# Performance work log

Measured on AMD Instinct MI355X. Metric: run time of the kernel, lower is better.

The kernel has to match this reference:

```python
import jax, jax.numpy as jnp
import numpy as np

FEAT = 1024     # args.gl_text_dim
BERT_DIM = 768
EPS = 1e-12     # torch F.normalize eps


def _conv_branch(x, W, b):
    # x: (bs, L, 768); W: (FEAT, K, 768); b: (FEAT,)
    # Equivalent to Conv2d(1, FEAT, (K, 768)) then relu, already transposed to (bs, L-K+1, FEAT)
    K = W.shape[1]
    L = x.shape[1]
    out = sum(jnp.einsum('bld,fd->blf', x[:, k:L - K + 1 + k, :], W[:, k, :]) for k in range(K))
    return jax.nn.relu(out + b)


def _l2norm(x, axis):
    n = jnp.sqrt(jnp.sum(x * x, axis=axis, keepdims=True))
    return x / jnp.maximum(n, EPS)


def setup_inputs() -> dict:
    key = jax.random.key(0)
    ks = jax.random.split(key, 10)
    bs, L = 128, 128
    def w(k, shape, fan_in):
        bound = 1.0 / np.sqrt(fan_in)
        return jax.random.uniform(k, shape, jnp.float32, -bound, bound)
    return {
        'words_emb': jax.random.normal(ks[0], (bs, L, BERT_DIM), jnp.float32),
        'sent_emb': jax.random.normal(ks[1], (bs, BERT_DIM), jnp.float32),
        'W2': w(ks[2], (FEAT, 2, BERT_DIM), 2 * BERT_DIM), 'b2': w(ks[3], (FEAT,), 2 * BERT_DIM),
        'W3': w(ks[4], (FEAT, 3, BERT_DIM), 3 * BERT_DIM), 'b3': w(ks[5], (FEAT,), 3 * BERT_DIM),
        'W4': w(ks[6], (FEAT, 4, BERT_DIM), 4 * BERT_DIM), 'b4': w(ks[7], (FEAT,), 4 * BERT_DIM),
        'Wp': w(ks[8], (FEAT, BERT_DIM), BERT_DIM), 'bp': w(ks[9], (FEAT,), BERT_DIM),
    }


def reference(words_emb, sent_emb, W2, b2, W3, b3, W4, b4, Wp, bp):
    # sentence head: dropout(eval=identity) -> linear -> l2 normalize
    sent = _l2norm(sent_emb @ Wp.T + bp, axis=-1)  # (bs, FEAT)

    L = words_emb.shape[1]  # == bert_words_num
    a = _conv_branch(words_emb, W2, b2)  # (bs, L-1, FEAT)
    b_ = _conv_branch(words_emb, W3, b3)  # (bs, L-2, FEAT)
    c = _conv_branch(words_emb, W4, b4)  # (bs, L-3, FEAT)

    seq = L - 1 - 3  # args.bert_words_num - 1 - 3
    main = jnp.maximum(jnp.maximum(a[:, :seq], b_[:, :seq]), c[:, :seq])  # (bs, seq, FEAT)
    pen = jnp.maximum(a[:, seq], b_[:, seq])[:, None]                      # (bs, 1, FEAT)
    last = a[:, seq + 1][:, None]                                          # (bs, 1, FEAT)
    code = jnp.concatenate([main, pen, last], axis=1)                      # (bs, L-2, FEAT)
    code = _l2norm(code, axis=2)
    words_out = jnp.transpose(code, (0, 2, 1))                             # (bs, FEAT, L-2)
    return words_out, sent
```

## Files before the change

kernel.cpp:

```cpp
#include <hip/hip_runtime.h>
#include <math.h>

typedef unsigned short u16;

#define BSZ 128
#define SEQL 128
#define DIM 768
#define FEAT 1024
#define WORDS_OUT_ELEMS (BSZ * FEAT * 126)

typedef __attribute__((ext_vector_type(8))) __bf16 bf16x8;
typedef __attribute__((ext_vector_type(4))) float f32x4;

__device__ __forceinline__ u16 f2bf(float x) {
  unsigned u = __float_as_uint(x);
  u += 0x7FFFu + ((u >> 16) & 1u);
  return (u16)(u >> 16);
}

__device__ __forceinline__ void gld_lds16(const void* g, void* l) {
  __builtin_amdgcn_global_load_lds(
      (const __attribute__((address_space(1))) void*)g,
      (__attribute__((address_space(3))) void*)l, 16, 0, 0);
}

#define N4_WORDS 3145728
#define N4_W2 393216
#define N4_W3 589824
#define N4_W4 786432
#define N4_TOTAL (N4_WORDS + N4_W2 + N4_W3 + N4_W4)

__global__ __launch_bounds__(256) void cvt_all(const float* __restrict__ words,
                                               const float* __restrict__ W2,
                                               const float* __restrict__ W3,
                                               const float* __restrict__ W4,
                                               u16* __restrict__ dA, u16* __restrict__ d2,
                                               u16* __restrict__ d3, u16* __restrict__ d4) {
  int i = blockIdx.x * 256 + threadIdx.x;
  if (i >= N4_TOTAL) return;
  const float* src;
  u16* dst;
  int j = i;
  if (j < N4_WORDS) {
    src = words; dst = dA;
  } else if ((j -= N4_WORDS) < N4_W2) {
    src = W2; dst = d2;
  } else if ((j -= N4_W2) < N4_W3) {
    src = W3; dst = d3;
  } else {
    j -= N4_W3; src = W4; dst = d4;
  }
  float4 v = ((const float4*)src)[j];
  ushort4 o;
  o.x = f2bf(v.x); o.y = f2bf(v.y); o.z = f2bf(v.z); o.w = f2bf(v.w);
  ((ushort4*)dst)[j] = o;
}

__device__ __forceinline__ void stage_tile(const u16* __restrict__ gbase, int stride,
                                           u16* __restrict__ ldsbase, int wave, int lane) {
#pragma unroll
  for (int i = 0; i < 4; ++i) {
    int slot = i * 256 + wave * 64 + lane;
    int r = slot >> 3, c = slot & 7;
    const u16* src = gbase + (size_t)r * stride + ((c ^ (r & 7)) * 8);
    unsigned uofs = __builtin_amdgcn_readfirstlane((unsigned)((i * 256 + wave * 64) * 8));
    gld_lds16(src, ldsbase + uofs);
  }
}

template <int K>
__device__ __forceinline__ void run_branch(const u16* __restrict__ A,
                                           const u16* __restrict__ W,
                                           const float* __restrict__ bias,
                                           u16* __restrict__ C,
                                           int b0, int tile_n, u16* lds) {
  const int KD = K * 768;
  const int Lp = 129 - K;
  const int tid = threadIdx.x;
  const int wave = tid >> 6, lane = tid & 63;
  u16* Xs = lds;
  u16* Wb0 = lds + 16384;
  u16* Wb1 = lds + 24576;

  const int bsel = wave & 1;
  const int wm = bsel * 128;
  const int wn = (wave >> 1) * 64;
  const int frow = lane & 15;
  const int fq = lane >> 4;

  const u16* xg0 = A + (size_t)b0 * 128 * 768;
  const u16* xg1 = A + (size_t)(b0 + 1) * 128 * 768;
  const u16* wg = W + (size_t)tile_n * 128 * KD;

  f32x4 acc[8][4];
#pragma unroll
  for (int mi = 0; mi < 8; ++mi)
#pragma unroll
    for (int ni = 0; ni < 4; ++ni) acc[mi][ni] = 0.0f;

  for (int d0 = 0; d0 < 768; d0 += 64) {
    stage_tile(xg0 + d0, 768, Xs, wave, lane);
    stage_tile(xg1 + d0, 768, Xs + 8192, wave, lane);
    stage_tile(wg + d0, KD, Wb0, wave, lane);
    __syncthreads();
#pragma unroll
    for (int k = 0; k < K; ++k) {
      if (k + 1 < K)
        stage_tile(wg + (k + 1) * 768 + d0, KD, ((k + 1) & 1) ? Wb1 : Wb0, wave, lane);
      const u16* wbuf = (k & 1) ? Wb1 : Wb0;
#pragma unroll
      for (int kc = 0; kc < 2; ++kc) {
        bf16x8 af[8], wf[4];
#pragma unroll
        for (int mi = 0; mi < 8; ++mi) {
          int row = wm + mi * 16 + frow + k;
          af[mi] = *(const bf16x8*)&Xs[(row * 8 + ((kc * 4 + fq) ^ (row & 7))) * 8];
        }
#pragma unroll
        for (int ni = 0; ni < 4; ++ni) {
          int row = wn + ni * 16 + frow;
          wf[ni] = *(const bf16x8*)&wbuf[(row * 8 + ((kc * 4 + fq) ^ (row & 7))) * 8];
        }
#pragma unroll
        for (int mi = 0; mi < 8; ++mi)
#pragma unroll
          for (int ni = 0; ni < 4; ++ni)
            acc[mi][ni] = __builtin_amdgcn_mfma_f32_16x16x32_bf16(af[mi], wf[ni],
                                                                  acc[mi][ni], 0, 0, 0);
      }
      __syncthreads();
    }
  }

  float bv[4];
#pragma unroll
  for (int ni = 0; ni < 4; ++ni) bv[ni] = bias[tile_n * 128 + wn + ni * 16 + frow];
  const int bb = b0 + bsel;
#pragma unroll
  for (int mi = 0; mi < 8; ++mi) {
#pragma unroll
    for (int r = 0; r < 4; ++r) {
      int mg = mi * 16 + fq * 4 + r;
      if (mg < Lp) {
        ushort4 hs;
        hs.x = f2bf(fmaxf(acc[mi][0][r] + bv[0], 0.0f));
        hs.y = f2bf(fmaxf(acc[mi][1][r] + bv[1], 0.0f));
        hs.z = f2bf(fmaxf(acc[mi][2][r] + bv[2], 0.0f));
        hs.w = f2bf(fmaxf(acc[mi][3][r] + bv[3], 0.0f));
        *(ushort4*)(C + (size_t)(bb * Lp + mg) * FEAT + tile_n * 128 + wn + frow * 4) = hs;
      }
    }
  }
}

__global__ __launch_bounds__(256, 2) void gemm_fused(const u16* __restrict__ A,
                                                     const u16* __restrict__ W2,
                                                     const u16* __restrict__ W3,
                                                     const u16* __restrict__ W4,
                                                     const float* __restrict__ b2,
                                                     const float* __restrict__ b3,
                                                     const float* __restrict__ b4,
                                                     u16* __restrict__ Ca,
                                                     u16* __restrict__ Cb,
                                                     u16* __restrict__ Cc) {
  __shared__ u16 lds[32768];
  const int tile_n = blockIdx.x;
  const int z = blockIdx.y;
  const int b0 = blockIdx.z * 2;
  if (z == 0)
    run_branch<2>(A, W2, b2, Ca, b0, tile_n, lds);
  else if (z == 1)
    run_branch<3>(A, W3, b3, Cb, b0, tile_n, lds);
  else
    run_branch<4>(A, W4, b4, Cc, b0, tile_n, lds);
}

__device__ __forceinline__ float4 load_bf4(const u16* p) {
  uint2 q = *(const uint2*)p;
  float4 r;
  r.x = __uint_as_float((q.x & 0xFFFFu) << 16);
  r.y = __uint_as_float(q.x & 0xFFFF0000u);
  r.z = __uint_as_float((q.y & 0xFFFFu) << 16);
  r.w = __uint_as_float(q.y & 0xFFFF0000u);
  return r;
}

#define CSTR 1028

__global__ __launch_bounds__(256) void combine_norm(const u16* __restrict__ a,
                                                    const u16* __restrict__ b,
                                                    const u16* __restrict__ c,
                                                    float* __restrict__ out) {
  __shared__ float comb[16 * CSTR];
  __shared__ float red[16 * 4];
  __shared__ float inv[16];
  const int tid = threadIdx.x;
  const int wave = tid >> 6, lane = tid & 63;
  const int l0 = blockIdx.x * 16;
  const int bb = blockIdx.y;
  const int rem = (126 - l0 < 16) ? (126 - l0) : 16;
  const int f0 = tid * 4;
  const int chunk = tid >> 4, frow = tid & 15;
  const int fbase = chunk * 64 + frow;

  float part[16];
#pragma unroll
  for (int l = 0; l < 16; ++l) {
    int lg = l0 + l;
    float4 v = make_float4(0.f, 0.f, 0.f, 0.f);
    if (lg < 126) {
      v = load_bf4(a + (size_t)(bb * 127 + lg) * 1024 + f0);
      if (lg < 125) {
        float4 vb = load_bf4(b + (size_t)(bb * 126 + lg) * 1024 + f0);
        v.x = fmaxf(v.x, vb.x); v.y = fmaxf(v.y, vb.y);
        v.z = fmaxf(v.z, vb.z); v.w = fmaxf(v.w, vb.w);
      }
      if (lg < 124) {
        float4 vc = load_bf4(c + (size_t)(bb * 125 + lg) * 1024 + f0);
        v.x = fmaxf(v.x, vc.x); v.y = fmaxf(v.y, vc.y);
        v.z = fmaxf(v.z, vc.z); v.w = fmaxf(v.w, vc.w);
      }
    }
    comb[l * CSTR + fbase + 0] = v.x;
    comb[l * CSTR + fbase + 16] = v.y;
    comb[l * CSTR + fbase + 32] = v.z;
    comb[l * CSTR + fbase + 48] = v.w;
    part[l] = v.x * v.x + v.y * v.y + v.z * v.z + v.w * v.w;
  }
#pragma unroll
  for (int l = 0; l < 16; ++l) {
    float v = part[l];
    for (int off = 32; off > 0; off >>= 1) v += __shfl_down(v, off);
    if (lane == 0) red[l * 4 + wave] = v;
  }
  __syncthreads();
  if (tid < 16) {
    float s = red[tid * 4] + red[tid * 4 + 1] + red[tid * 4 + 2] + red[tid * 4 + 3];
    inv[tid] = 1.0f / fmaxf(sqrtf(s), 1e-12f);
  }
  __syncthreads();

  const int q = lane & 3, fi = lane >> 2;
  const int lb = 4 * q;
  const size_t ob = (size_t)bb * FEAT * 126;
#pragma unroll
  for (int it = 0; it < 16; ++it) {
    int f = wave * 256 + it * 16 + fi;
    if (lb + 2 <= rem) {
      float* po = out + ob + (size_t)f * 126 + l0 + lb;
      float2 w0;
      w0.x = comb[(lb + 0) * CSTR + f] * inv[lb + 0];
      w0.y = comb[(lb + 1) * CSTR + f] * inv[lb + 1];
      *(float2*)po = w0;
      if (lb + 4 <= rem) {
        float2 w1;
        w1.x = comb[(lb + 2) * CSTR + f] * inv[lb + 2];
        w1.y = comb[(lb + 3) * CSTR + f] * inv[lb + 3];
        *(float2*)(po + 2) = w1;
      }
    }
  }
}

__global__ __launch_bounds__(256) void sent_head(const float* __restrict__ se,
                                                 const float* __restrict__ Wp,
                                                 const float* __restrict__ bp,
                                                 float* __restrict__ out) {
  __shared__ float srow[768];
  __shared__ float ov[1024];
  __shared__ float red[4];
  const int b = blockIdx.x, tid = threadIdx.x;
  for (int i = tid; i < 768; i += 256) srow[i] = se[b * 768 + i];
  __syncthreads();
  float ss = 0.f;
#pragma unroll
  for (int it = 0; it < 4; ++it) {
    int f = tid + it * 256;
    const float4* w = (const float4*)(Wp + (size_t)f * 768);
    float acc = 0.f;
    for (int j = 0; j < 192; ++j) {
      float4 wv = w[j];
      float4 sv = *(const float4*)&srow[j * 4];
      acc += wv.x * sv.x + wv.y * sv.y + wv.z * sv.z + wv.w * sv.w;
    }
    acc += bp[f];
    ov[f] = acc;
    ss += acc * acc;
  }
  const int lane = tid & 63, wave = tid >> 6;
  for (int off = 32; off > 0; off >>= 1) ss += __shfl_down(ss, off);
  if (lane == 0) red[wave] = ss;
  __syncthreads();
  float tot = red[0] + red[1] + red[2] + red[3];
  float inv = 1.0f / fmaxf(sqrtf(tot), 1e-12f);
  for (int it = 0; it < 4; ++it) {
    int f = tid + it * 256;
    out[WORDS_OUT_ELEMS + (size_t)b * 1024 + f] = ov[f] * inv;
  }
}

extern "C" void kernel_launch(void* const* d_in, const int* in_sizes, int n_in,
                              void* d_out, int out_size, void* d_ws, size_t ws_size,
                              hipStream_t stream) {
  const float* words = (const float*)d_in[0];
  const float* sent = (const float*)d_in[1];
  const float* W2 = (const float*)d_in[2];
  const float* b2 = (const float*)d_in[3];
  const float* W3 = (const float*)d_in[4];
  const float* b3 = (const float*)d_in[5];
  const float* W4 = (const float*)d_in[6];
  const float* b4 = (const float*)d_in[7];
  const float* Wp = (const float*)d_in[8];
  const float* bp = (const float*)d_in[9];
  float* out = (float*)d_out;

  char* ws = (char*)d_ws;
  u16* A_bf = (u16*)(ws + 0);
  u16* W2_bf = (u16*)(ws + 25165824);
  u16* W3_bf = (u16*)(ws + 28311552);
  u16* W4_bf = (u16*)(ws + 33030144);
  u16* a_out = (u16*)(ws + 39321600);
  u16* b_out = (u16*)(ws + 72613888);
  u16* c_out = (u16*)(ws + 105644032);

  cvt_all<<<(N4_TOTAL + 255) / 256, 256, 0, stream>>>(words, W2, W3, W4,
                                                      A_bf, W2_bf, W3_bf, W4_bf);

  gemm_fused<<<dim3(8, 3, BSZ / 2), 256, 0, stream>>>(A_bf, W2_bf, W3_bf, W4_bf,
                                                      b2, b3, b4, a_out, b_out, c_out);

  combine_norm<<<dim3(8, BSZ), 256, 0, stream>>>(a_out, b_out, c_out, out);
  sent_head<<<BSZ, 256, 0, stream>>>(sent, Wp, bp, out);
}
```

Baseline: 476.7 us.

## Enlarge conv GEMM tile to four batches per block with double-buffered X

Each block now covers four batch items, one per wave, with each wave holding a 128x128 output tile (8x8 MFMA fragments), where before each wave held 128x64. The X staging is double-buffered across the d-chunk loop, and the W stages form one continuous ping-pong pipeline across (d, k) steps. The goal is to halve W traffic per output and overlap X loads with compute. In exchange, LDS use rises to 160KB and accumulator registers double, dropping occupancy to one block per CU, and the grid shrinks to 768 blocks.

Result: slower. 690.9 us (+44.9%).

```diff
diff --git a/kernel.cpp b/kernel.cpp
--- a/kernel.cpp
+++ b/kernel.cpp
@@ -78,53 +78,65 @@
   const int Lp = 129 - K;
   const int tid = threadIdx.x;
   const int wave = tid >> 6, lane = tid & 63;
-  u16* Xs = lds;
-  u16* Wb0 = lds + 16384;
-  u16* Wb1 = lds + 24576;
-
-  const int bsel = wave & 1;
-  const int wm = bsel * 128;
-  const int wn = (wave >> 1) * 64;
+  u16* Xb0 = lds;
+  u16* Xb1 = lds + 32768;
+  u16* Wb0 = lds + 65536;
+  u16* Wb1 = lds + 73728;
+
   const int frow = lane & 15;
   const int fq = lane >> 4;
 
-  const u16* xg0 = A + (size_t)b0 * 128 * 768;
-  const u16* xg1 = A + (size_t)(b0 + 1) * 128 * 768;
+  const u16* xg = A + (size_t)b0 * 98304;
   const u16* wg = W + (size_t)tile_n * 128 * KD;
 
-  f32x4 acc[8][4];
+  f32x4 acc[8][8];
 #pragma unroll
   for (int mi = 0; mi < 8; ++mi)
 #pragma unroll
-    for (int ni = 0; ni < 4; ++ni) acc[mi][ni] = 0.0f;
-
-  for (int d0 = 0; d0 < 768; d0 += 64) {
-    stage_tile(xg0 + d0, 768, Xs, wave, lane);
-    stage_tile(xg1 + d0, 768, Xs + 8192, wave, lane);
-    stage_tile(wg + d0, KD, Wb0, wave, lane);
-    __syncthreads();
+    for (int ni = 0; ni < 8; ++ni) acc[mi][ni] = 0.0f;
+
+#pragma unroll
+  for (int q = 0; q < 4; ++q)
+    stage_tile(xg + (size_t)q * 98304, 768, Xb0 + q * 8192, wave, lane);
+  stage_tile(wg, KD, Wb0, wave, lane);
+  __syncthreads();
+
+  for (int d0i = 0; d0i < 12; ++d0i) {
+    const int dd = d0i * 64;
+    u16* Xcur = (d0i & 1) ? Xb1 : Xb0;
 #pragma unroll
     for (int k = 0; k < K; ++k) {
-      if (k + 1 < K)
-        stage_tile(wg + (k + 1) * 768 + d0, KD, ((k + 1) & 1) ? Wb1 : Wb0, wave, lane);
-      const u16* wbuf = (k & 1) ? Wb1 : Wb0;
+      const int s = d0i * K + k;
+      if (s + 1 < 12 * K) {
+        const int nk = (k + 1 < K) ? k + 1 : 0;
+        const int nd = (k + 1 < K) ? dd : dd + 64;
+        stage_tile(wg + nk * 768 + nd, KD, ((s + 1) & 1) ? Wb1 : Wb0, wave, lane);
+      }
+      if (k == K - 1 && d0i < 11) {
+        u16* Xn = (d0i & 1) ? Xb0 : Xb1;
+#pragma unroll
+        for (int q = 0; q < 4; ++q)
+          stage_tile(xg + (size_t)q * 98304 + dd + 64, 768, Xn + q * 8192, wave, lane);
+      }
+      const u16* xb = Xcur + wave * 8192;
+      const u16* wb = (s & 1) ? Wb1 : Wb0;
 #pragma unroll
       for (int kc = 0; kc < 2; ++kc) {
-        bf16x8 af[8], wf[4];
+        bf16x8 af[8], wf[8];
 #pragma unroll
         for (int mi = 0; mi < 8; ++mi) {
-          int row = wm + mi * 16 + frow + k;
-          af[mi] = *(const bf16x8*)&Xs[(row * 8 + ((kc * 4 + fq) ^ (row & 7))) * 8];
+          int row = mi * 16 + frow + k;
+          af[mi] = *(const bf16x8*)&xb[(row * 8 + ((kc * 4 + fq) ^ (row & 7))) * 8];
         }
 #pragma unroll
-        for (int ni = 0; ni < 4; ++ni) {
-          int row = wn + ni * 16 + frow;
-          wf[ni] = *(const bf16x8*)&wbuf[(row * 8 + ((kc * 4 + fq) ^ (row & 7))) * 8];
+        for (int ni = 0; ni < 8; ++ni) {
+          int row = ni * 16 + frow;
+          wf[ni] = *(const bf16x8*)&wb[(row * 8 + ((kc * 4 + fq) ^ (row & 7))) * 8];
         }
 #pragma unroll
         for (int mi = 0; mi < 8; ++mi)
 #pragma unroll
-          for (int ni = 0; ni < 4; ++ni)
+          for (int ni = 0; ni < 8; ++ni)
             acc[mi][ni] = __builtin_amdgcn_mfma_f32_16x16x32_bf16(af[mi], wf[ni],
                                                                   acc[mi][ni], 0, 0, 0);
       }
@@ -132,28 +144,34 @@
     }
   }
 
-  float bv[4];
-#pragma unroll
-  for (int ni = 0; ni < 4; ++ni) bv[ni] = bias[tile_n * 128 + wn + ni * 16 + frow];
-  const int bb = b0 + bsel;
+  float bv[8];
+#pragma unroll
+  for (int ni = 0; ni < 8; ++ni) bv[ni] = bias[tile_n * 128 + ni * 16 + frow];
+  const int bb = b0 + wave;
 #pragma unroll
   for (int mi = 0; mi < 8; ++mi) {
 #pragma unroll
     for (int r = 0; r < 4; ++r) {
       int mg = mi * 16 + fq * 4 + r;
       if (mg < Lp) {
-        ushort4 hs;
-        hs.x = f2bf(fmaxf(acc[mi][0][r] + bv[0], 0.0f));
-        hs.y = f2bf(fmaxf(acc[mi][1][r] + bv[1], 0.0f));
-        hs.z = f2bf(fmaxf(acc[mi][2][r] + bv[2], 0.0f));
-        hs.w = f2bf(fmaxf(acc[mi][3][r] + bv[3], 0.0f));
-        *(ushort4*)(C + (size_t)(bb * Lp + mg) * FEAT + tile_n * 128 + wn + frow * 4) = hs;
-      }
-    }
-  }
-}
-
-__global__ __launch_bounds__(256, 2) void gemm_fused(const u16* __restrict__ A,
+        ushort4 h0, h1;
+        h0.x = f2bf(fmaxf(acc[mi][0][r] + bv[0], 0.0f));
+        h0.y = f2bf(fmaxf(acc[mi][1][r] + bv[1], 0.0f));
+        h0.z = f2bf(fmaxf(acc[mi][2][r] + bv[2], 0.0f));
+        h0.w = f2bf(fmaxf(acc[mi][3][r] + bv[3], 0.0f));
+        h1.x = f2bf(fmaxf(acc[mi][4][r] + bv[4], 0.0f));
+        h1.y = f2bf(fmaxf(acc[mi][5][r] + bv[5], 0.0f));
+        h1.z = f2bf(fmaxf(acc[mi][6][r] + bv[6], 0.0f));
+        h1.w = f2bf(fmaxf(acc[mi][7][r] + bv[7], 0.0f));
+        u16* pc = C + (size_t)(bb * Lp + mg) * FEAT + tile_n * 128;
+        *(ushort4*)(pc + frow * 4) = h0;
+        *(ushort4*)(pc + 64 + frow * 4) = h1;
+      }
+    }
+  }
+}
+
+__global__ __launch_bounds__(256, 1) void gemm_fused(const u16* __restrict__ A,
                                                      const u16* __restrict__ W2,
                                                      const u16* __restrict__ W3,
                                                      const u16* __restrict__ W4,
@@ -163,10 +181,10 @@
                                                      u16* __restrict__ Ca,
                                                      u16* __restrict__ Cb,
                                                      u16* __restrict__ Cc) {
-  __shared__ u16 lds[32768];
+  __shared__ u16 lds[81920];
   const int tile_n = blockIdx.x;
   const int z = blockIdx.y;
-  const int b0 = blockIdx.z * 2;
+  const int b0 = blockIdx.z * 4;
   if (z == 0)
     run_branch<2>(A, W2, b2, Ca, b0, tile_n, lds);
   else if (z == 1)
@@ -326,7 +344,7 @@
   cvt_all<<<(N4_TOTAL + 255) / 256, 256, 0, stream>>>(words, W2, W3, W4,
                                                       A_bf, W2_bf, W3_bf, W4_bf);
 
-  gemm_fused<<<dim3(8, 3, BSZ / 2), 256, 0, stream>>>(A_bf, W2_bf, W3_bf, W4_bf,
+  gemm_fused<<<dim3(8, 3, BSZ / 4), 256, 0, stream>>>(A_bf, W2_bf, W3_bf, W4_bf,
                                                       b2, b3, b4, a_out, b_out, c_out);
 
   combine_norm<<<dim3(8, BSZ), 256, 0, stream>>>(a_out, b_out, c_out, out);
```

## Enlarge GEMM block to four batches with double-buffered X/W LDS pipeline

Applied to the files above, without the earlier changes.

The conv-GEMM block now covers four batch items with 512 threads, and the launch grid is halved along z. It stages the whole 64-wide X slice for all four batches into a double buffer and prefetches the next slice and the next W tile during compute. Waits now use explicit vmcnt counts and split MFMA phases with setprio and s_barrier instead of full __syncthreads. This aims to reuse each W tile across more rows and overlap global-to-LDS loads with MFMA work. The cost is 160KB of LDS per block, which allows one block per CU, plus fragile hand-tuned wait counts.

New measurement: 503.0 us. 1.06x slower.

```diff
diff --git a/kernel.cpp b/kernel.cpp
--- a/kernel.cpp
+++ b/kernel.cpp
@@ -23,6 +23,10 @@
       (const __attribute__((address_space(1))) void*)g,
       (__attribute__((address_space(3))) void*)l, 16, 0, 0);
 }
+
+#define WAITVM0 asm volatile("s_waitcnt vmcnt(0)" ::: "memory")
+#define WAITVM2 asm volatile("s_waitcnt vmcnt(2)" ::: "memory")
+#define WAITVM4 asm volatile("s_waitcnt vmcnt(4)" ::: "memory")
 
 #define N4_WORDS 3145728
 #define N4_W2 393216
@@ -56,17 +60,40 @@
   ((ushort4*)dst)[j] = o;
 }
 
-__device__ __forceinline__ void stage_tile(const u16* __restrict__ gbase, int stride,
-                                           u16* __restrict__ ldsbase, int wave, int lane) {
-#pragma unroll
-  for (int i = 0; i < 4; ++i) {
-    int slot = i * 256 + wave * 64 + lane;
+__device__ __forceinline__ void stage_tile512(const u16* __restrict__ gbase, int stride,
+                                              u16* __restrict__ ldsbase, int wave, int lane) {
+#pragma unroll
+  for (int p = 0; p < 2; ++p) {
+    int slot = p * 512 + wave * 64 + lane;
     int r = slot >> 3, c = slot & 7;
     const u16* src = gbase + (size_t)r * stride + ((c ^ (r & 7)) * 8);
-    unsigned uofs = __builtin_amdgcn_readfirstlane((unsigned)((i * 256 + wave * 64) * 8));
+    unsigned uofs = __builtin_amdgcn_readfirstlane((unsigned)((p * 512 + wave * 64) * 8));
     gld_lds16(src, ldsbase + uofs);
   }
 }
+
+#define GPHASE(kc, mh, WLOAD)                                                        \
+  {                                                                                  \
+    bf16x8 af[4];                                                                    \
+    _Pragma("unroll") for (int i = 0; i < 4; ++i) {                                  \
+      int row = (mh * 4 + i) * 16 + frow + k;                                        \
+      af[i] = *(const bf16x8*)&xb[(row * 8 + ((kc * 4 + fq) ^ (row & 7))) * 8];      \
+    }                                                                                \
+    if (WLOAD) {                                                                     \
+      _Pragma("unroll") for (int ni = 0; ni < 4; ++ni) {                             \
+        int row = wn + ni * 16 + frow;                                               \
+        wf[ni] = *(const bf16x8*)&wcur[(row * 8 + ((kc * 4 + fq) ^ (row & 7))) * 8]; \
+      }                                                                              \
+    }                                                                                \
+    __builtin_amdgcn_s_setprio(1);                                                   \
+    _Pragma("unroll") for (int i = 0; i < 4; ++i)                                    \
+        _Pragma("unroll") for (int ni = 0; ni < 4; ++ni)                             \
+            acc[mh * 4 + i][ni] = __builtin_amdgcn_mfma_f32_16x16x32_bf16(           \
+                af[i], wf[ni], acc[mh * 4 + i][ni], 0, 0, 0);                        \
+    __builtin_amdgcn_s_setprio(0);                                                   \
+    __builtin_amdgcn_sched_barrier(0);                                               \
+    __builtin_amdgcn_s_barrier();                                                    \
+  }
 
 template <int K>
 __device__ __forceinline__ void run_branch(const u16* __restrict__ A,
@@ -76,20 +103,15 @@
                                            int b0, int tile_n, u16* lds) {
   const int KD = K * 768;
   const int Lp = 129 - K;
+  const int S = 12 * K;
   const int tid = threadIdx.x;
   const int wave = tid >> 6, lane = tid & 63;
-  u16* Xs = lds;
-  u16* Wb0 = lds + 16384;
-  u16* Wb1 = lds + 24576;
-
-  const int bsel = wave & 1;
-  const int wm = bsel * 128;
-  const int wn = (wave >> 1) * 64;
   const int frow = lane & 15;
   const int fq = lane >> 4;
-
-  const u16* xg0 = A + (size_t)b0 * 128 * 768;
-  const u16* xg1 = A + (size_t)(b0 + 1) * 128 * 768;
+  const int wq = wave >> 1;
+  const int wn = (wave & 1) * 64;
+
+  const u16* xg = A + (size_t)b0 * 98304;
   const u16* wg = W + (size_t)tile_n * 128 * KD;
 
   f32x4 acc[8][4];
@@ -98,44 +120,50 @@
 #pragma unroll
     for (int ni = 0; ni < 4; ++ni) acc[mi][ni] = 0.0f;
 
-  for (int d0 = 0; d0 < 768; d0 += 64) {
-    stage_tile(xg0 + d0, 768, Xs, wave, lane);
-    stage_tile(xg1 + d0, 768, Xs + 8192, wave, lane);
-    stage_tile(wg + d0, KD, Wb0, wave, lane);
-    __syncthreads();
+#pragma unroll
+  for (int q = 0; q < 4; ++q)
+    stage_tile512(xg + (size_t)q * 98304, 768, lds + q * 8192, wave, lane);
+  stage_tile512(wg, KD, lds + 65536, wave, lane);
+  WAITVM0;
+  __builtin_amdgcn_sched_barrier(0);
+  __syncthreads();
+
+  for (int d0i = 0; d0i < 12; ++d0i) {
+    const int dd = d0i * 64;
+    u16* Xcur = (d0i & 1) ? (lds + 32768) : lds;
+    u16* Xnxt = (d0i & 1) ? lds : (lds + 32768);
+    const u16* xb = Xcur + wq * 8192;
 #pragma unroll
     for (int k = 0; k < K; ++k) {
-      if (k + 1 < K)
-        stage_tile(wg + (k + 1) * 768 + d0, KD, ((k + 1) & 1) ? Wb1 : Wb0, wave, lane);
-      const u16* wbuf = (k & 1) ? Wb1 : Wb0;
-#pragma unroll
-      for (int kc = 0; kc < 2; ++kc) {
-        bf16x8 af[8], wf[4];
-#pragma unroll
-        for (int mi = 0; mi < 8; ++mi) {
-          int row = wm + mi * 16 + frow + k;
-          af[mi] = *(const bf16x8*)&Xs[(row * 8 + ((kc * 4 + fq) ^ (row & 7))) * 8];
-        }
-#pragma unroll
-        for (int ni = 0; ni < 4; ++ni) {
-          int row = wn + ni * 16 + frow;
-          wf[ni] = *(const bf16x8*)&wbuf[(row * 8 + ((kc * 4 + fq) ^ (row & 7))) * 8];
-        }
-#pragma unroll
-        for (int mi = 0; mi < 8; ++mi)
-#pragma unroll
-          for (int ni = 0; ni < 4; ++ni)
-            acc[mi][ni] = __builtin_amdgcn_mfma_f32_16x16x32_bf16(af[mi], wf[ni],
-                                                                  acc[mi][ni], 0, 0, 0);
-      }
-      __syncthreads();
+      const int s = d0i * K + k;
+      const bool lastk = (k == K - 1);
+      const bool stx = lastk && (d0i < 11);
+      u16* wcur = (s & 1) ? (lds + 73728) : (lds + 65536);
+      u16* wnxt = (s & 1) ? (lds + 65536) : (lds + 73728);
+      const int nk = lastk ? 0 : k + 1;
+      const int nd = lastk ? dd + 64 : dd;
+
+      if (s + 1 < S) stage_tile512(wg + nk * 768 + nd, KD, wnxt, wave, lane);
+      if (stx) stage_tile512(xg + dd + 64, 768, Xnxt, wave, lane);
+      if (s + 1 == S) { WAITVM0; } else if (stx) { WAITVM4; } else { WAITVM2; }
+      __builtin_amdgcn_sched_barrier(0);
+      __builtin_amdgcn_s_barrier();
+
+      bf16x8 wf[4];
+      GPHASE(0, 0, 1)
+      if (stx) stage_tile512(xg + 98304 + dd + 64, 768, Xnxt + 8192, wave, lane);
+      GPHASE(0, 1, 0)
+      if (stx) stage_tile512(xg + 2 * 98304 + dd + 64, 768, Xnxt + 16384, wave, lane);
+      GPHASE(1, 0, 1)
+      if (stx) stage_tile512(xg + (size_t)3 * 98304 + dd + 64, 768, Xnxt + 24576, wave, lane);
+      GPHASE(1, 1, 0)
     }
   }
 
   float bv[4];
 #pragma unroll
   for (int ni = 0; ni < 4; ++ni) bv[ni] = bias[tile_n * 128 + wn + ni * 16 + frow];
-  const int bb = b0 + bsel;
+  const int bb = b0 + wq;
 #pragma unroll
   for (int mi = 0; mi < 8; ++mi) {
 #pragma unroll
@@ -153,7 +181,7 @@
   }
 }
 
-__global__ __launch_bounds__(256, 2) void gemm_fused(const u16* __restrict__ A,
+__global__ __launch_bounds__(512, 1) void gemm_fused(const u16* __restrict__ A,
                                                      const u16* __restrict__ W2,
                                                      const u16* __restrict__ W3,
                                                      const u16* __restrict__ W4,
@@ -163,10 +191,10 @@
                                                      u16* __restrict__ Ca,
                                                      u16* __restrict__ Cb,
                                                      u16* __restrict__ Cc) {
-  __shared__ u16 lds[32768];
+  __shared__ u16 lds[81920];
   const int tile_n = blockIdx.x;
   const int z = blockIdx.y;
-  const int b0 = blockIdx.z * 2;
+  const int b0 = blockIdx.z * 4;
   if (z == 0)
     run_branch<2>(A, W2, b2, Ca, b0, tile_n, lds);
   else if (z == 1)
@@ -326,7 +354,7 @@
   cvt_all<<<(N4_TOTAL + 255) / 256, 256, 0, stream>>>(words, W2, W3, W4,
                                                       A_bf, W2_bf, W3_bf, W4_bf);
 
-  gemm_fused<<<dim3(8, 3, BSZ / 2), 256, 0, stream>>>(A_bf, W2_bf, W3_bf, W4_bf,
+  gemm_fused<<<dim3(8, 3, BSZ / 4), 512, 0, stream>>>(A_bf, W2_bf, W3_bf, W4_bf,
                                                       b2, b3, b4, a_out, b_out, c_out);
 
   combine_norm<<<dim3(8, BSZ), 256, 0, stream>>>(a_out, b_out, c_out, out);
```

## Restructure conv GEMM: 4 batches per block, double-buffered X, weights via registers

Applied to the files above, without the earlier changes.

The GEMM kernel now uses 512-thread blocks covering four batch items, with the X tiles double-buffered in LDS so the next d-slice is loaded while the current one is computed. Weight fragments are no longer staged through LDS. Each wave loads them straight from global memory into registers and prefetches the next k-slice's fragments during the MFMAs. Wave priority is raised around the MFMA bursts, and there is one barrier per d-slice instead of one per k. The aim is to cut barrier count and LDS staging of weights and to hide load latency. The cost is higher register pressure, uncoalesced global weight reads, and one block per CU with about 132KB of LDS.

Result: slower. 703.4 us (+47.6%).

```diff
diff --git a/kernel.cpp b/kernel.cpp
--- a/kernel.cpp
+++ b/kernel.cpp
@@ -23,6 +23,8 @@
       (const __attribute__((address_space(1))) void*)g,
       (__attribute__((address_space(3))) void*)l, 16, 0, 0);
 }
+
+#define WAITVM0 asm volatile("s_waitcnt vmcnt(0)" ::: "memory")
 
 #define N4_WORDS 3145728
 #define N4_W2 393216
@@ -56,14 +58,14 @@
   ((ushort4*)dst)[j] = o;
 }
 
-__device__ __forceinline__ void stage_tile(const u16* __restrict__ gbase, int stride,
-                                           u16* __restrict__ ldsbase, int wave, int lane) {
-#pragma unroll
-  for (int i = 0; i < 4; ++i) {
-    int slot = i * 256 + wave * 64 + lane;
+__device__ __forceinline__ void stage_tile512(const u16* __restrict__ gbase, int stride,
+                                              u16* __restrict__ ldsbase, int wave, int lane) {
+#pragma unroll
+  for (int p = 0; p < 2; ++p) {
+    int slot = p * 512 + wave * 64 + lane;
     int r = slot >> 3, c = slot & 7;
     const u16* src = gbase + (size_t)r * stride + ((c ^ (r & 7)) * 8);
-    unsigned uofs = __builtin_amdgcn_readfirstlane((unsigned)((i * 256 + wave * 64) * 8));
+    unsigned uofs = __builtin_amdgcn_readfirstlane((unsigned)((p * 512 + wave * 64) * 8));
     gld_lds16(src, ldsbase + uofs);
   }
 }
@@ -78,19 +80,17 @@
   const int Lp = 129 - K;
   const int tid = threadIdx.x;
   const int wave = tid >> 6, lane = tid & 63;
-  u16* Xs = lds;
-  u16* Wb0 = lds + 16384;
-  u16* Wb1 = lds + 24576;
-
-  const int bsel = wave & 1;
-  const int wm = bsel * 128;
-  const int wn = (wave >> 1) * 64;
   const int frow = lane & 15;
   const int fq = lane >> 4;
-
-  const u16* xg0 = A + (size_t)b0 * 128 * 768;
-  const u16* xg1 = A + (size_t)(b0 + 1) * 128 * 768;
+  const int wq = wave >> 1;
+  const int wn = (wave & 1) * 64;
+
+  const u16* xg = A + (size_t)b0 * 98304;
   const u16* wg = W + (size_t)tile_n * 128 * KD;
+  const u16* pW[4];
+#pragma unroll
+  for (int ni = 0; ni < 4; ++ni)
+    pW[ni] = wg + (size_t)(wn + ni * 16 + frow) * KD + fq * 8;
 
   f32x4 acc[8][4];
 #pragma unroll
@@ -98,44 +98,70 @@
 #pragma unroll
     for (int ni = 0; ni < 4; ++ni) acc[mi][ni] = 0.0f;
 
-  for (int d0 = 0; d0 < 768; d0 += 64) {
-    stage_tile(xg0 + d0, 768, Xs, wave, lane);
-    stage_tile(xg1 + d0, 768, Xs + 8192, wave, lane);
-    stage_tile(wg + d0, KD, Wb0, wave, lane);
+#pragma unroll
+  for (int q = 0; q < 4; ++q)
+    stage_tile512(xg + (size_t)q * 98304, 768, lds + q * 8192, wave, lane);
+  bf16x8 wf[8];
+#pragma unroll
+  for (int kc = 0; kc < 2; ++kc)
+#pragma unroll
+    for (int ni = 0; ni < 4; ++ni)
+      wf[kc * 4 + ni] = *(const bf16x8*)(pW[ni] + kc * 32);
+  WAITVM0;
+  __builtin_amdgcn_sched_barrier(0);
+  __syncthreads();
+
+  for (int d0i = 0; d0i < 12; ++d0i) {
+    const int dd = d0i * 64;
+    u16* Xcur = (d0i & 1) ? (lds + 32768) : lds;
+    u16* Xnxt = (d0i & 1) ? lds : (lds + 32768);
+    const u16* xb = Xcur + wq * 8192;
+    if (d0i < 11) {
+#pragma unroll
+      for (int q = 0; q < 4; ++q)
+        stage_tile512(xg + (size_t)q * 98304 + dd + 64, 768, Xnxt + q * 8192, wave, lane);
+    }
+#pragma unroll
+    for (int k = 0; k < K; ++k) {
+      bf16x8 wfn[8];
+      const bool havenext = (k + 1 < K) || (d0i < 11);
+      if (havenext) {
+        const int noff = (k + 1 < K) ? ((k + 1) * 768 + dd) : dd + 64;
+#pragma unroll
+        for (int kc = 0; kc < 2; ++kc)
+#pragma unroll
+          for (int ni = 0; ni < 4; ++ni)
+            wfn[kc * 4 + ni] = *(const bf16x8*)(pW[ni] + noff + kc * 32);
+      }
+#pragma unroll
+      for (int kc = 0; kc < 2; ++kc) {
+        bf16x8 af[8];
+#pragma unroll
+        for (int mi = 0; mi < 8; ++mi) {
+          int row = mi * 16 + frow + k;
+          af[mi] = *(const bf16x8*)&xb[(row * 8 + ((kc * 4 + fq) ^ (row & 7))) * 8];
+        }
+        __builtin_amdgcn_s_setprio(1);
+#pragma unroll
+        for (int mi = 0; mi < 8; ++mi)
+#pragma unroll
+          for (int ni = 0; ni < 4; ++ni)
+            acc[mi][ni] = __builtin_amdgcn_mfma_f32_16x16x32_bf16(af[mi], wf[kc * 4 + ni],
+                                                                  acc[mi][ni], 0, 0, 0);
+        __builtin_amdgcn_s_setprio(0);
+      }
+      if (havenext) {
+#pragma unroll
+        for (int j = 0; j < 8; ++j) wf[j] = wfn[j];
+      }
+    }
     __syncthreads();
-#pragma unroll
-    for (int k = 0; k < K; ++k) {
-      if (k + 1 < K)
-        stage_tile(wg + (k + 1) * 768 + d0, KD, ((k + 1) & 1) ? Wb1 : Wb0, wave, lane);
-      const u16* wbuf = (k & 1) ? Wb1 : Wb0;
-#pragma unroll
-      for (int kc = 0; kc < 2; ++kc) {
-        bf16x8 af[8], wf[4];
-#pragma unroll
-        for (int mi = 0; mi < 8; ++mi) {
-          int row = wm + mi * 16 + frow + k;
-          af[mi] = *(const bf16x8*)&Xs[(row * 8 + ((kc * 4 + fq) ^ (row & 7))) * 8];
-        }
-#pragma unroll
-        for (int ni = 0; ni < 4; ++ni) {
-          int row = wn + ni * 16 + frow;
-          wf[ni] = *(const bf16x8*)&wbuf[(row * 8 + ((kc * 4 + fq) ^ (row & 7))) * 8];
-        }
-#pragma unroll
-        for (int mi = 0; mi < 8; ++mi)
-#pragma unroll
-          for (int ni = 0; ni < 4; ++ni)
-            acc[mi][ni] = __builtin_amdgcn_mfma_f32_16x16x32_bf16(af[mi], wf[ni],
-                                                                  acc[mi][ni], 0, 0, 0);
-      }
-      __syncthreads();
-    }
   }
 
   float bv[4];
 #pragma unroll
   for (int ni = 0; ni < 4; ++ni) bv[ni] = bias[tile_n * 128 + wn + ni * 16 + frow];
-  const int bb = b0 + bsel;
+  const int bb = b0 + wq;
 #pragma unroll
   for (int mi = 0; mi < 8; ++mi) {
 #pragma unroll
@@ -153,7 +179,7 @@
   }
 }
 
-__global__ __launch_bounds__(256, 2) void gemm_fused(const u16* __restrict__ A,
+__global__ __launch_bounds__(512, 1) void gemm_fused(const u16* __restrict__ A,
                                                      const u16* __restrict__ W2,
                                                      const u16* __restrict__ W3,
                                                      const u16* __restrict__ W4,
@@ -163,10 +189,10 @@
                                                      u16* __restrict__ Ca,
                                                      u16* __restrict__ Cb,
                                                      u16* __restrict__ Cc) {
-  __shared__ u16 lds[32768];
+  __shared__ u16 lds[67584];
   const int tile_n = blockIdx.x;
   const int z = blockIdx.y;
-  const int b0 = blockIdx.z * 2;
+  const int b0 = blockIdx.z * 4;
   if (z == 0)
     run_branch<2>(A, W2, b2, Ca, b0, tile_n, lds);
   else if (z == 1)
@@ -326,7 +352,7 @@
   cvt_all<<<(N4_TOTAL + 255) / 256, 256, 0, stream>>>(words, W2, W3, W4,
                                                       A_bf, W2_bf, W3_bf, W4_bf);
 
-  gemm_fused<<<dim3(8, 3, BSZ / 2), 256, 0, stream>>>(A_bf, W2_bf, W3_bf, W4_bf,
+  gemm_fused<<<dim3(8, 3, BSZ / 4), 512, 0, stream>>>(A_bf, W2_bf, W3_bf, W4_bf,
                                                       b2, b3, b4, a_out, b_out, c_out);
 
   combine_norm<<<dim3(8, BSZ), 256, 0, stream>>>(a_out, b_out, c_out, out);
```
